# Kernel tuning notes

Measured on AMD Instinct MI355X. Metric: run time of the kernel, lower is better.

## Reference

```python
import jax, jax.numpy as jnp
import numpy as np

WS = 16          # window_size
OWS = 24         # overlap_win_size = int(ws*0.5) + ws
PAD = (OWS - WS) // 2
NH = 6           # num_heads


def _ln(x, g, b):
    m = jnp.mean(x, axis=-1, keepdims=True)
    v = jnp.mean((x - m) ** 2, axis=-1, keepdims=True)
    return (x - m) * jax.lax.rsqrt(v + 1e-5) * g + b


def setup_inputs() -> dict:
    key = jax.random.key(0)
    ks = jax.random.split(key, 12)
    B, H, W, C = 4, 64, 64, 180
    std = 0.02
    x = jax.random.normal(ks[0], (B, H * W, C), jnp.float32)
    y = jax.random.normal(ks[1], (B, H * W, C), jnp.float32)
    kv_w = jax.random.normal(ks[2], (2 * C, C), jnp.float32) * std
    kv_b = jnp.zeros((2 * C,), jnp.float32)
    q_w = jax.random.normal(ks[3], (C, C), jnp.float32) * std
    q_b = jnp.zeros((C,), jnp.float32)
    rpb = jax.random.normal(ks[4], ((WS + OWS - 1) ** 2, NH), jnp.float32) * std
    proj_w = jax.random.normal(ks[5], (C, C), jnp.float32) * std
    proj_b = jnp.zeros((C,), jnp.float32)
    fc1_w = jax.random.normal(ks[6], (4 * C, C), jnp.float32) * std
    fc1_b = jnp.zeros((4 * C,), jnp.float32)
    fc2_w = jax.random.normal(ks[7], (C, 4 * C), jnp.float32) * std
    fc2_b = jnp.zeros((C,), jnp.float32)
    norm1_g = jnp.ones((C,), jnp.float32); norm1_b = jnp.zeros((C,), jnp.float32)
    norm2_g = jnp.ones((C,), jnp.float32); norm2_b = jnp.zeros((C,), jnp.float32)
    # relative position index (HAT-style OCA): query coords vs extended window coords
    co = np.stack(np.meshgrid(np.arange(WS), np.arange(WS), indexing='ij')).reshape(2, -1)   # 2, ws*ws
    ce = np.stack(np.meshgrid(np.arange(OWS), np.arange(OWS), indexing='ij')).reshape(2, -1) # 2, ows*ows
    rel = (ce[:, None, :] - co[:, :, None]).transpose(1, 2, 0) + (WS - 1)  # nq, n, 2 in [0, ws+ows-2]
    rpi = jnp.asarray(rel[..., 0] * (WS + OWS - 1) + rel[..., 1], jnp.int32)  # [256, 576]
    return {
        'x': x, 'y': y,
        'norm1_g': norm1_g, 'norm1_b': norm1_b,
        'kv_w': kv_w, 'kv_b': kv_b, 'q_w': q_w, 'q_b': q_b,
        'rpb': rpb, 'proj_w': proj_w, 'proj_b': proj_b,
        'norm2_g': norm2_g, 'norm2_b': norm2_b,
        'fc1_w': fc1_w, 'fc1_b': fc1_b, 'fc2_w': fc2_w, 'fc2_b': fc2_b,
        'rpi': rpi, 'h': 64, 'w': 64,
    }


def reference(x, y, norm1_g, norm1_b, kv_w, kv_b, q_w, q_b, rpb, proj_w, proj_b,
              norm2_g, norm2_b, fc1_w, fc1_b, fc2_w, fc2_b, rpi, h, w):
    b, L, c = x.shape
    nh = NH
    d = c // nh
    scale = d ** -0.5
    nwh, nww = h // WS, w // WS
    nq, n = WS * WS, OWS * OWS

    shortcut = x
    xn = _ln(x, norm1_g, norm1_b).reshape(b, h, w, c)
    yn = _ln(y, norm1_g, norm1_b).reshape(b, h, w, c)

    kv = xn @ kv_w.T + kv_b                                  # b,h,w,2c
    q = yn @ q_w.T + q_b                                     # b,h,w,c

    # kv -> [2, b, c, h, w] then pad spatially and extract overlapping windows (nn.Unfold)
    kv = kv.reshape(b, h, w, 2, c).transpose(3, 0, 4, 1, 2)  # 2,b,c,h,w
    kvp = jnp.pad(kv, ((0, 0), (0, 0), (0, 0), (PAD, PAD), (PAD, PAD)))
    hh = jnp.arange(nwh)[:, None] * WS + jnp.arange(OWS)[None, :]   # [nwh, OWS]
    ww = jnp.arange(nww)[:, None] * WS + jnp.arange(OWS)[None, :]   # [nww, OWS]
    patches = kvp[:, :, :, hh][:, :, :, :, :, ww]            # 2,b,c,nwh,OWS,nww,OWS
    kvw = patches.transpose(0, 1, 3, 5, 4, 6, 2).reshape(2, b * nwh * nww, n, c)
    kwin, vwin = kvw[0], kvw[1]                              # [b_, n, c]

    # non-overlapping query windows (window_partition)
    qwin = q.reshape(b, nwh, WS, nww, WS, c).transpose(0, 1, 3, 2, 4, 5).reshape(-1, nq, c)
    b_ = qwin.shape[0]

    qh = qwin.reshape(b_, nq, nh, d).transpose(0, 2, 1, 3) * scale
    kh = kwin.reshape(b_, n, nh, d).transpose(0, 2, 1, 3)
    vh = vwin.reshape(b_, n, nh, d).transpose(0, 2, 1, 3)

    attn = jnp.einsum('bhqd,bhkd->bhqk', qh, kh)             # [b_, nh, nq, n]
    bias = rpb[rpi.reshape(-1)].reshape(nq, n, nh).transpose(2, 0, 1)  # [nh, nq, n]
    attn = jax.nn.softmax(attn + bias[None], axis=-1)
    out = jnp.einsum('bhqk,bhkd->bhqd', attn, vh).transpose(0, 2, 1, 3).reshape(b_, nq, c)

    # window_reverse
    out = out.reshape(b, nwh, nww, WS, WS, c).transpose(0, 1, 3, 2, 4, 5).reshape(b, h * w, c)

    xo = out @ proj_w.T + proj_b + shortcut
    xn2 = _ln(xo, norm2_g, norm2_b)
    mlp = jax.nn.gelu(xn2 @ fc1_w.T + fc1_b, approximate=False) @ fc2_w.T + fc2_b
    return xo + mlp
```

## Files before the change

kernel.cpp:

```cpp
#include <hip/hip_runtime.h>

typedef __bf16 bf16;
typedef __bf16 bf16x8 __attribute__((ext_vector_type(8)));
typedef __bf16 bf16x4 __attribute__((ext_vector_type(4)));
typedef __bf16 bf16x2 __attribute__((ext_vector_type(2)));
typedef float f32x4 __attribute__((ext_vector_type(4)));

static __device__ __forceinline__ bf16x8 ld8(const bf16* p) {
    return *reinterpret_cast<const bf16x8*>(p);
}
static __device__ __forceinline__ bf16x4 ld4(const bf16* p) {
    return *reinterpret_cast<const bf16x4*>(p);
}
static __device__ __forceinline__ bf16x8 ld8_b32(const bf16* p) {
    bf16x8 v;
#pragma unroll
    for (int i = 0; i < 4; ++i) {
        bf16x2 t = *reinterpret_cast<const bf16x2*>(p + i * 2);
        v[i * 2] = t[0]; v[i * 2 + 1] = t[1];
    }
    return v;
}
static __device__ __forceinline__ bf16x8 zero8() {
    bf16x8 v;
#pragma unroll
    for (int i = 0; i < 8; ++i) v[i] = (bf16)0.f;
    return v;
}

#define MFMA16(a, b, c) __builtin_amdgcn_mfma_f32_16x16x32_bf16((a), (b), (c), 0, 0, 0)

template <int BK, int KPAD>
static __device__ __forceinline__ void stage_tile(const bf16* __restrict__ g,
                                                  bf16* __restrict__ lds, int tid) {
    constexpr int CPR = BK / 8;
    constexpr int NP = 64 * CPR / 256;
#pragma unroll
    for (int p = 0; p < NP; ++p) {
        int idx = p * 256 + tid;
        int row = idx / CPR, cg = idx % CPR;
        bf16x8 v = ld8(g + (long)row * KPAD + cg * 8);
        *reinterpret_cast<bf16x8*>(lds + row * 200 + cg * 8) = v;
    }
}
template <int BK, int KPAD>
static __device__ __forceinline__ void load_chunk(const bf16* __restrict__ g,
                                                  bf16x8* r, int tid) {
    constexpr int CPR = BK / 8;
    constexpr int NP = 64 * CPR / 256;
#pragma unroll
    for (int p = 0; p < NP; ++p) {
        int idx = p * 256 + tid;
        int row = idx / CPR, cg = idx % CPR;
        r[p] = ld8(g + (long)row * KPAD + cg * 8);
    }
}
template <int BK>
static __device__ __forceinline__ void store_chunk(bf16* __restrict__ lds,
                                                   const bf16x8* r, int tid) {
    constexpr int CPR = BK / 8;
    constexpr int NP = 64 * CPR / 256;
#pragma unroll
    for (int p = 0; p < NP; ++p) {
        int idx = p * 256 + tid;
        int row = idx / CPR, cg = idx % CPR;
        *reinterpret_cast<bf16x8*>(lds + row * 200 + cg * 8) = r[p];
    }
}

__global__ __launch_bounds__(256) void prep_kernel(
    const float* __restrict__ kv_w, const float* __restrict__ q_w,
    const float* __restrict__ proj_w, const float* __restrict__ fc1_w,
    const float* __restrict__ fc2_w, const float* __restrict__ rpb,
    const int* __restrict__ rpi,
    bf16* __restrict__ wkv, bf16* __restrict__ wq, bf16* __restrict__ wproj,
    bf16* __restrict__ wfc1, bf16* __restrict__ wfc2, bf16* __restrict__ biast)
{
    int i = blockIdx.x * 256 + threadIdx.x;
    if (i < 73728) {
        int n = i / 192, k = i % 192;
        float v = (n < 360 && k < 180) ? kv_w[n * 180 + k] : 0.f;
        wkv[i] = (bf16)v;
    } else if (i < 122880) {
        int j = i - 73728; int n = j / 192, k = j % 192;
        float v = (n < 180 && k < 180) ? q_w[n * 180 + k] : 0.f;
        wq[j] = (bf16)v;
    } else if (i < 172032) {
        int j = i - 122880; int n = j / 192, k = j % 192;
        int hh = k >> 5, d = k & 31;
        float v = (n < 180 && d < 30) ? proj_w[n * 180 + hh * 30 + d] : 0.f;
        wproj[j] = (bf16)v;
    } else if (i < 319488) {
        int j = i - 172032; int n = j / 192, k = j % 192;
        float v = (n < 720 && k < 180) ? fc1_w[n * 180 + k] : 0.f;
        wfc1[j] = (bf16)v;
    } else if (i < 507904) {
        int j = i - 319488; int n = j / 736, k = j % 736;
        float v = (n < 180 && k < 720) ? fc2_w[n * 720 + k] : 0.f;
        wfc2[j] = (bf16)v;
    } else if (i < 1392640) {
        int t = i - 507904;
        int r = t & 3;
        int lane = (t >> 2) & 63;
        int tmp2 = t >> 8;
        int kg = tmp2 % 36;
        int tmp3 = tmp2 / 36;
        int qg = tmp3 & 15;
        int h = tmp3 >> 4;
        int q = qg * 16 + (lane & 15);
        int key = kg * 16 + ((lane >> 4) << 2) + r;
        biast[t] = (bf16)rpb[rpi[q * 576 + key] * 6 + h];
    }
}

__global__ __launch_bounds__(256) void ln_kernel(
    const float* __restrict__ srcA, const float* __restrict__ srcB,
    const float* __restrict__ g, const float* __restrict__ b,
    bf16* __restrict__ dst)
{
    int wave = threadIdx.x >> 6, lane = threadIdx.x & 63;
    int row = blockIdx.x * 4 + wave;
    const float* sp = (row < 16384) ? (srcA + row * 180) : (srcB + (row - 16384) * 180);
    float v0 = sp[lane];
    float v1 = sp[lane + 64];
    float v2 = (lane < 52) ? sp[lane + 128] : 0.f;
    float s = v0 + v1 + v2;
    float sq = v0 * v0 + v1 * v1 + v2 * v2;
#pragma unroll
    for (int m = 32; m >= 1; m >>= 1) {
        s += __shfl_xor(s, m);
        sq += __shfl_xor(sq, m);
    }
    float mean = s * (1.f / 180.f);
    float var = sq * (1.f / 180.f) - mean * mean;
    float rs = rsqrtf(var + 1e-5f);
    bf16* dp = dst + (long)row * 192;
    dp[lane] = (bf16)((v0 - mean) * rs * g[lane] + b[lane]);
    dp[lane + 64] = (bf16)((v1 - mean) * rs * g[lane + 64] + b[lane + 64]);
    float o2 = (lane < 52) ? ((v2 - mean) * rs * g[lane + 128] + b[lane + 128]) : 0.f;
    dp[lane + 128] = (bf16)o2;
}

__global__ __launch_bounds__(256, 4) void gemm_kvq(
    const bf16* __restrict__ xn, const bf16* __restrict__ yn,
    const bf16* __restrict__ wkv, const bf16* __restrict__ wq,
    const float* __restrict__ kv_b, const float* __restrict__ q_b,
    bf16* __restrict__ kvbuf, bf16* __restrict__ qbuf)
{
    const int tid = threadIdx.x, wave = tid >> 6, lane = tid & 63;
    const int llo = lane & 15, quad = lane >> 4;
    const int bz = blockIdx.y;
    const bool isq = (bz == 2);
    const bf16* A = isq ? yn : xn;
    const bf16* Wbase = isq ? wq : (wkv + (long)bz * 3 * 64 * 192);
    const int tm = blockIdx.x * 64;

    __shared__ __align__(16) bf16 Sa[64 * 200];
    __shared__ __align__(16) bf16 Sb[64 * 200];

    stage_tile<192, 192>(A + (long)tm * 192, Sa, tid);
    bf16x8 wreg[6];
    load_chunk<192, 192>(Wbase, wreg, tid);

    for (int s = 0; s < 3; ++s) {
        if (s) __syncthreads();
        store_chunk<192>(Sb, wreg, tid);
        __syncthreads();
        if (s < 2) load_chunk<192, 192>(Wbase + (long)(s + 1) * 64 * 192, wreg, tid);

        f32x4 acc[4];
#pragma unroll
        for (int nt = 0; nt < 4; ++nt)
#pragma unroll
            for (int r = 0; r < 4; ++r) acc[nt][r] = 0.f;
#pragma unroll
        for (int kt = 0; kt < 6; ++kt) {
            bf16x8 a = ld8(Sa + (wave * 16 + llo) * 200 + kt * 32 + quad * 8);
#pragma unroll
            for (int nt = 0; nt < 4; ++nt) {
                bf16x8 b = ld8(Sb + (nt * 16 + llo) * 200 + kt * 32 + quad * 8);
                acc[nt] = MFMA16(a, b, acc[nt]);
            }
        }

        const int g = bz * 3 + s;
#pragma unroll
        for (int nt = 0; nt < 4; ++nt)
#pragma unroll
            for (int r = 0; r < 4; ++r) {
                int m = tm + wave * 16 + quad * 4 + r;
                int n = g * 64 + nt * 16 + llo;
                if (!isq) {
                    if (n < 360) {
                        float v = acc[nt][r] + kv_b[n];
                        int nn = n % 180;
                        int col = (n / 180) * 192 + (nn / 30) * 32 + (nn % 30);
                        kvbuf[(long)m * 384 + col] = (bf16)v;
                    }
                } else {
                    int nq = n - 384;
                    if (nq < 180) {
                        float v = (acc[nt][r] + q_b[nq]) * 0.18257418583505537f;
                        int col = (nq / 30) * 32 + (nq % 30);
                        qbuf[(long)m * 192 + col] = (bf16)v;
                    }
                }
            }
    }
}

__global__ __launch_bounds__(512, 6) void attn_kernel(
    const bf16* __restrict__ qbuf,
    const bf16* __restrict__ kvbuf,
    const bf16* __restrict__ biast,
    bf16* __restrict__ obuf)
{
    const int qhalf = blockIdx.x & 1;
    const int head = (blockIdx.x >> 1) % 6;
    const int win = blockIdx.x / 12;
    const int bb = win / 16, wi = (win % 16) / 4, wj = win % 4;
    const int tid = threadIdx.x;
    const int wave = tid >> 6, lane = tid & 63;
    const int llo = lane & 15, quad = lane >> 4;
    const int qbase = qhalf * 128 + wave * 16;
    const int qg = qhalf * 8 + wave;

    __shared__ bf16 Kc[2][64][40];
    __shared__ bf16 Vt[2][32][74];
    __shared__ bf16 Ps[8][16][72];

    const int u = tid & 255;
    const int tloc = u >> 2, dq = u & 3;
    const bool isV = tid >= 256;
    int aa = tloc / 24, w0 = tloc % 24;

    const int q0 = qbase + llo;
    const int gr_q = bb * 4096 + (wi * 16 + (q0 >> 4)) * 64 + (wj * 16 + (q0 & 15));
    const bf16x8 qf = ld8(qbuf + (long)gr_q * 192 + head * 32 + quad * 8);
    const bf16* bbase = biast + ((long)(head * 16 + qg) * 36) * 256 + lane * 4;

    {
        int gy = wi * 16 + aa - 4, gx = wj * 16 + w0 - 4;
        bf16x8 st = zero8();
        if ((unsigned)gy < 64u && (unsigned)gx < 64u) {
            long gr = (long)(bb * 4096 + gy * 64 + gx) * 384;
            st = ld8(kvbuf + gr + (isV ? 192 : 0) + head * 32 + dq * 8);
        }
        if (!isV) {
            *reinterpret_cast<bf16x8*>(&Kc[0][tloc][dq * 8]) = st;
        } else {
#pragma unroll
            for (int j = 0; j < 8; ++j) Vt[0][dq * 8 + j][tloc] = st[j];
        }
    }
    __syncthreads();

    f32x4 o[2];
    float m_run = -1e30f, l_run = 0.f;
#pragma unroll
    for (int n2 = 0; n2 < 2; ++n2)
#pragma unroll
        for (int r = 0; r < 4; ++r) o[n2][r] = 0.f;

    for (int c = 0; c < 9; ++c) {
        const int cur = c & 1;

        bf16x8 stage;
        if (c < 8) {
            w0 += 16; aa += 2;
            if (w0 >= 24) { w0 -= 24; ++aa; }
            int gy = wi * 16 + aa - 4, gx = wj * 16 + w0 - 4;
            stage = zero8();
            if ((unsigned)gy < 64u && (unsigned)gx < 64u) {
                long gr = (long)(bb * 4096 + gy * 64 + gx) * 384;
                stage = ld8(kvbuf + gr + (isV ? 192 : 0) + head * 32 + dq * 8);
            }
        }

        f32x4 s[4];
#pragma unroll
        for (int kt = 0; kt < 4; ++kt) {
            bf16x8 kf = ld8(&Kc[cur][kt * 16 + llo][quad * 8]);
            f32x4 zc;
            zc[0] = 0.f; zc[1] = 0.f; zc[2] = 0.f; zc[3] = 0.f;
            s[kt] = MFMA16(kf, qf, zc);
        }

#pragma unroll
        for (int kt = 0; kt < 4; ++kt) {
            bf16x4 bv = ld4(bbase + (c * 4 + kt) * 256);
#pragma unroll
            for (int r = 0; r < 4; ++r) s[kt][r] += (float)bv[r];
        }

        float mx = s[0][0];
#pragma unroll
        for (int kt = 0; kt < 4; ++kt)
#pragma unroll
            for (int r = 0; r < 4; ++r) mx = fmaxf(mx, s[kt][r]);
        mx = fmaxf(mx, __shfl_xor(mx, 16));
        mx = fmaxf(mx, __shfl_xor(mx, 32));
        float m_new = fmaxf(m_run, mx);
        float alpha = __expf(m_run - m_new);
        float ls = 0.f;
#pragma unroll
        for (int kt = 0; kt < 4; ++kt)
#pragma unroll
            for (int r = 0; r < 4; ++r) {
                float p = __expf(s[kt][r] - m_new);
                s[kt][r] = p;
                ls += p;
            }
        ls += __shfl_xor(ls, 16);
        ls += __shfl_xor(ls, 32);
        l_run = l_run * alpha + ls;
        m_run = m_new;

#pragma unroll
        for (int r = 0; r < 4; ++r) {
            float a = __shfl(alpha, quad * 4 + r);
            o[0][r] *= a;
            o[1][r] *= a;
        }

#pragma unroll
        for (int kt = 0; kt < 4; ++kt) {
            bf16x4 pv;
#pragma unroll
            for (int r = 0; r < 4; ++r) pv[r] = (bf16)s[kt][r];
            *reinterpret_cast<bf16x4*>(&Ps[wave][llo][kt * 16 + quad * 4]) = pv;
        }

#pragma unroll
        for (int kt2 = 0; kt2 < 2; ++kt2) {
            bf16x8 pa = ld8(&Ps[wave][llo][kt2 * 32 + quad * 8]);
#pragma unroll
            for (int n2 = 0; n2 < 2; ++n2) {
                bf16x8 vb = ld8_b32(&Vt[cur][n2 * 16 + llo][kt2 * 32 + quad * 8]);
                o[n2] = MFMA16(pa, vb, o[n2]);
            }
        }

        if (c < 8) {
            if (!isV) {
                *reinterpret_cast<bf16x8*>(&Kc[1 - cur][tloc][dq * 8]) = stage;
            } else {
#pragma unroll
                for (int j = 0; j < 8; ++j) Vt[1 - cur][dq * 8 + j][tloc] = stage[j];
            }
            __syncthreads();
        }
    }

    float linv = 1.f / l_run;
#pragma unroll
    for (int r = 0; r < 4; ++r) {
        float li = __shfl(linv, quad * 4 + r);
        int q = qbase + quad * 4 + r;
        int gr = bb * 4096 + (wi * 16 + (q >> 4)) * 64 + (wj * 16 + (q & 15));
#pragma unroll
        for (int n2 = 0; n2 < 2; ++n2)
            obuf[(long)gr * 192 + head * 32 + n2 * 16 + llo] = (bf16)(o[n2][r] * li);
    }
}

__global__ __launch_bounds__(256, 3) void gemm_projln(
    const bf16* __restrict__ obuf, const bf16* __restrict__ wproj,
    const float* __restrict__ proj_b, const float* __restrict__ x,
    const float* __restrict__ g, const float* __restrict__ bln,
    float* __restrict__ xo, bf16* __restrict__ xn2)
{
    const int tid = threadIdx.x, wave = tid >> 6, lane = tid & 63;
    const int llo = lane & 15, quad = lane >> 4;
    const int mbase = blockIdx.x * 64;

    __shared__ __align__(16) bf16 Sa[64 * 200];
    __shared__ __align__(16) bf16 Sb[64 * 200];
    stage_tile<192, 192>(obuf + (long)mbase * 192, Sa, tid);
    bf16x8 wreg[6];
    load_chunk<192, 192>(wproj, wreg, tid);

    f32x4 acc[12];
#pragma unroll
    for (int nt = 0; nt < 12; ++nt)
#pragma unroll
        for (int r = 0; r < 4; ++r) acc[nt][r] = 0.f;

    for (int nc = 0; nc < 3; ++nc) {
        if (nc) __syncthreads();
        store_chunk<192>(Sb, wreg, tid);
        __syncthreads();
        if (nc < 2) load_chunk<192, 192>(wproj + (long)(nc + 1) * 64 * 192, wreg, tid);
#pragma unroll
        for (int kt = 0; kt < 6; ++kt) {
            bf16x8 a = ld8(Sa + (wave * 16 + llo) * 200 + kt * 32 + quad * 8);
#pragma unroll
            for (int nt = 0; nt < 4; ++nt) {
                bf16x8 b = ld8(Sb + (nt * 16 + llo) * 200 + kt * 32 + quad * 8);
                acc[nc * 4 + nt] = MFMA16(a, b, acc[nc * 4 + nt]);
            }
        }
    }

#pragma unroll
    for (int r = 0; r < 4; ++r) {
        int m = mbase + wave * 16 + quad * 4 + r;
        float v[12];
        float sum = 0.f, sq = 0.f;
#pragma unroll
        for (int nt = 0; nt < 12; ++nt) {
            int n = nt * 16 + llo;
            float val = 0.f;
            if (n < 180) val = acc[nt][r] + proj_b[n] + x[(long)m * 180 + n];
            v[nt] = val;
            sum += val; sq += val * val;
        }
#pragma unroll
        for (int msk = 1; msk <= 8; msk <<= 1) {
            sum += __shfl_xor(sum, msk);
            sq  += __shfl_xor(sq, msk);
        }
        float mean = sum * (1.f / 180.f);
        float var = sq * (1.f / 180.f) - mean * mean;
        float rs = rsqrtf(var + 1e-5f);
#pragma unroll
        for (int nt = 0; nt < 12; ++nt) {
            int n = nt * 16 + llo;
            if (n < 180) {
                xo[(long)m * 180 + n] = v[nt];
                xn2[(long)m * 192 + n] = (bf16)((v[nt] - mean) * rs * g[n] + bln[n]);
            } else {
                xn2[(long)m * 192 + n] = (bf16)0.f;
            }
        }
    }
}

__global__ __launch_bounds__(256, 4) void gemm_fc1(
    const bf16* __restrict__ A, const bf16* __restrict__ W,
    const float* __restrict__ bias, bf16* __restrict__ outp)
{
    const int tid = threadIdx.x, wave = tid >> 6, lane = tid & 63;
    const int llo = lane & 15, quad = lane >> 4;
    const int tm = blockIdx.x * 64;
    const int bz = blockIdx.y;
    const bf16* Wbase = W + (long)bz * 3 * 64 * 192;

    __shared__ __align__(16) bf16 Sa[64 * 200];
    __shared__ __align__(16) bf16 Sb[64 * 200];
    stage_tile<192, 192>(A + (long)tm * 192, Sa, tid);
    bf16x8 wreg[6];
    load_chunk<192, 192>(Wbase, wreg, tid);

    for (int s = 0; s < 3; ++s) {
        if (s) __syncthreads();
        store_chunk<192>(Sb, wreg, tid);
        __syncthreads();
        if (s < 2) load_chunk<192, 192>(Wbase + (long)(s + 1) * 64 * 192, wreg, tid);

        f32x4 acc[4];
#pragma unroll
        for (int nt = 0; nt < 4; ++nt)
#pragma unroll
            for (int r = 0; r < 4; ++r) acc[nt][r] = 0.f;
#pragma unroll
        for (int kt = 0; kt < 6; ++kt) {
            bf16x8 a = ld8(Sa + (wave * 16 + llo) * 200 + kt * 32 + quad * 8);
#pragma unroll
            for (int nt = 0; nt < 4; ++nt) {
                bf16x8 b = ld8(Sb + (nt * 16 + llo) * 200 + kt * 32 + quad * 8);
                acc[nt] = MFMA16(a, b, acc[nt]);
            }
        }

        const int nb = (bz * 3 + s) * 64;
#pragma unroll
        for (int nt = 0; nt < 4; ++nt)
#pragma unroll
            for (int r = 0; r < 4; ++r) {
                int m = tm + wave * 16 + quad * 4 + r;
                int n = nb + nt * 16 + llo;
                if (n >= 720) continue;
                float v = acc[nt][r] + bias[n];
                float gel = 0.5f * v * (1.f + erff(v * 0.7071067811865475f));
                outp[(long)m * 736 + n] = (bf16)gel;
            }
    }
}

__global__ __launch_bounds__(256, 4) void gemm_fc2(
    const bf16* __restrict__ A, const bf16* __restrict__ W,
    const float* __restrict__ bias, const float* __restrict__ resid,
    float* __restrict__ outp)
{
    const int tid = threadIdx.x, wave = tid >> 6, lane = tid & 63;
    const int llo = lane & 15, quad = lane >> 4;
    const int tm = blockIdx.x * 64;
    const int tn = blockIdx.y * 64;

    __shared__ __align__(16) bf16 Sa[64 * 200];
    __shared__ __align__(16) bf16 Sb[64 * 200];

    const bf16* Ap = A + (long)tm * 736;
    const bf16* Wp = W + (long)tn * 736;

    bf16x8 ar[6], wr[6];
    load_chunk<192, 736>(Ap, ar, tid);
    load_chunk<192, 736>(Wp, wr, tid);

    f32x4 acc[4];
#pragma unroll
    for (int nt = 0; nt < 4; ++nt)
#pragma unroll
        for (int r = 0; r < 4; ++r) acc[nt][r] = 0.f;

#pragma unroll
    for (int c = 0; c < 4; ++c) {
        if (c) __syncthreads();
        if (c < 3) { store_chunk<192>(Sa, ar, tid); store_chunk<192>(Sb, wr, tid); }
        else       { store_chunk<160>(Sa, ar, tid); store_chunk<160>(Sb, wr, tid); }
        __syncthreads();
        if (c < 2) {
            load_chunk<192, 736>(Ap + (c + 1) * 192, ar, tid);
            load_chunk<192, 736>(Wp + (c + 1) * 192, wr, tid);
        } else if (c == 2) {
            load_chunk<160, 736>(Ap + 576, ar, tid);
            load_chunk<160, 736>(Wp + 576, wr, tid);
        }
        const int nkt = (c == 3) ? 5 : 6;
        for (int kt = 0; kt < nkt; ++kt) {
            bf16x8 a = ld8(Sa + (wave * 16 + llo) * 200 + kt * 32 + quad * 8);
#pragma unroll
            for (int nt = 0; nt < 4; ++nt) {
                bf16x8 b = ld8(Sb + (nt * 16 + llo) * 200 + kt * 32 + quad * 8);
                acc[nt] = MFMA16(a, b, acc[nt]);
            }
        }
    }

#pragma unroll
    for (int nt = 0; nt < 4; ++nt)
#pragma unroll
        for (int r = 0; r < 4; ++r) {
            int m = tm + wave * 16 + quad * 4 + r;
            int n = tn + nt * 16 + llo;
            if (n >= 180) continue;
            float v = acc[nt][r] + bias[n];
            outp[(long)m * 180 + n] = v + resid[(long)m * 180 + n];
        }
}

extern "C" void kernel_launch(void* const* d_in, const int* in_sizes, int n_in,
                              void* d_out, int out_size, void* d_ws, size_t ws_size,
                              hipStream_t stream) {
    const float* x      = (const float*)d_in[0];
    const float* y      = (const float*)d_in[1];
    const float* n1g    = (const float*)d_in[2];
    const float* n1b    = (const float*)d_in[3];
    const float* kv_w   = (const float*)d_in[4];
    const float* kv_b   = (const float*)d_in[5];
    const float* q_w    = (const float*)d_in[6];
    const float* q_b    = (const float*)d_in[7];
    const float* rpb    = (const float*)d_in[8];
    const float* proj_w = (const float*)d_in[9];
    const float* proj_b = (const float*)d_in[10];
    const float* n2g    = (const float*)d_in[11];
    const float* n2b    = (const float*)d_in[12];
    const float* fc1_w  = (const float*)d_in[13];
    const float* fc1_b  = (const float*)d_in[14];
    const float* fc2_w  = (const float*)d_in[15];
    const float* fc2_b  = (const float*)d_in[16];
    const int*   rpi    = (const int*)d_in[17];

    char* ws = (char*)d_ws;
    bf16* xn    = (bf16*)(ws + 0);
    bf16* yn    = (bf16*)(ws + 6291456);
    bf16* qbuf  = (bf16*)(ws + 12582912);
    bf16* kvbuf = (bf16*)(ws + 18874368);
    bf16* obuf  = (bf16*)(ws + 31457280);
    float* xo   = (float*)(ws + 37748736);
    bf16* biast = (bf16*)(ws + 49545216);
    bf16* wkv   = (bf16*)(ws + 51314688);
    bf16* wq    = (bf16*)(ws + 51462144);
    bf16* wproj = (bf16*)(ws + 51560448);
    bf16* wfc1  = (bf16*)(ws + 51658752);
    bf16* wfc2  = (bf16*)(ws + 51953664);
    bf16* hmid  = (bf16*)(ws + 6291456);
    bf16* xn2   = xn;

    prep_kernel<<<5440, 256, 0, stream>>>(kv_w, q_w, proj_w, fc1_w, fc2_w, rpb, rpi,
                                          wkv, wq, wproj, wfc1, wfc2, biast);
    ln_kernel<<<8192, 256, 0, stream>>>(x, y, n1g, n1b, xn);
    gemm_kvq<<<dim3(256, 3), 256, 0, stream>>>(xn, yn, wkv, wq, kv_b, q_b, kvbuf, qbuf);
    attn_kernel<<<768, 512, 0, stream>>>(qbuf, kvbuf, biast, obuf);
    gemm_projln<<<256, 256, 0, stream>>>(obuf, wproj, proj_b, x, n2g, n2b, xo, xn2);
    gemm_fc1<<<dim3(256, 4), 256, 0, stream>>>(xn2, wfc1, fc1_b, hmid);
    gemm_fc2<<<dim3(256, 3), 256, 0, stream>>>(hmid, wfc2, fc2_b, xo, (float*)d_out);
}
```

Before: 211.9 us.

## Fuse LN into prep kernel and double M-tile for kvq and fc1 GEMMs

Merges the weight/bias prep kernel and the first layernorm kernel into one launch, removing a kernel launch. The kvq and fc1 GEMMs now use 512-thread blocks with 128-row A tiles, so each staged weight chunk is reused across twice as many rows and grid size halves. Bias loads in the epilogues are hoisted out of the per-row loop. The larger LDS footprint per block may lower occupancy.

```diff
diff --git a/kernel.cpp b/kernel.cpp
--- a/kernel.cpp
+++ b/kernel.cpp
@@ -30,45 +30,54 @@
 
 #define MFMA16(a, b, c) __builtin_amdgcn_mfma_f32_16x16x32_bf16((a), (b), (c), 0, 0, 0)
 
-template <int BK, int KPAD>
+template <int ROWS, int BK, int KPAD, int THREADS>
+static __device__ __forceinline__ void load_chunk_g(const bf16* __restrict__ g,
+                                                    bf16x8* r, int tid) {
+    constexpr int TOT = ROWS * BK / 8;
+    constexpr int NP = (TOT + THREADS - 1) / THREADS;
+#pragma unroll
+    for (int p = 0; p < NP; ++p) {
+        int idx = p * THREADS + tid;
+        if ((TOT % THREADS) == 0 || idx < TOT) {
+            int row = idx / (BK / 8), cg = idx % (BK / 8);
+            r[p] = ld8(g + (long)row * KPAD + cg * 8);
+        }
+    }
+}
+template <int ROWS, int BK, int THREADS>
+static __device__ __forceinline__ void store_chunk_l(bf16* __restrict__ lds,
+                                                     const bf16x8* r, int tid) {
+    constexpr int TOT = ROWS * BK / 8;
+    constexpr int NP = (TOT + THREADS - 1) / THREADS;
+#pragma unroll
+    for (int p = 0; p < NP; ++p) {
+        int idx = p * THREADS + tid;
+        if ((TOT % THREADS) == 0 || idx < TOT) {
+            int row = idx / (BK / 8), cg = idx % (BK / 8);
+            *reinterpret_cast<bf16x8*>(lds + row * 200 + cg * 8) = r[p];
+        }
+    }
+}
+template <int ROWS, int BK, int KPAD, int THREADS>
 static __device__ __forceinline__ void stage_tile(const bf16* __restrict__ g,
                                                   bf16* __restrict__ lds, int tid) {
-    constexpr int CPR = BK / 8;
-    constexpr int NP = 64 * CPR / 256;
+    constexpr int TOT = ROWS * BK / 8;
+    constexpr int NP = (TOT + THREADS - 1) / THREADS;
 #pragma unroll
     for (int p = 0; p < NP; ++p) {
-        int idx = p * 256 + tid;
-        int row = idx / CPR, cg = idx % CPR;
-        bf16x8 v = ld8(g + (long)row * KPAD + cg * 8);
-        *reinterpret_cast<bf16x8*>(lds + row * 200 + cg * 8) = v;
-    }
-}
-template <int BK, int KPAD>
-static __device__ __forceinline__ void load_chunk(const bf16* __restrict__ g,
-                                                  bf16x8* r, int tid) {
-    constexpr int CPR = BK / 8;
-    constexpr int NP = 64 * CPR / 256;
-#pragma unroll
-    for (int p = 0; p < NP; ++p) {
-        int idx = p * 256 + tid;
-        int row = idx / CPR, cg = idx % CPR;
-        r[p] = ld8(g + (long)row * KPAD + cg * 8);
-    }
-}
-template <int BK>
-static __device__ __forceinline__ void store_chunk(bf16* __restrict__ lds,
-                                                   const bf16x8* r, int tid) {
-    constexpr int CPR = BK / 8;
-    constexpr int NP = 64 * CPR / 256;
-#pragma unroll
-    for (int p = 0; p < NP; ++p) {
-        int idx = p * 256 + tid;
-        int row = idx / CPR, cg = idx % CPR;
-        *reinterpret_cast<bf16x8*>(lds + row * 200 + cg * 8) = r[p];
-    }
-}
-
-__global__ __launch_bounds__(256) void prep_kernel(
+        int idx = p * THREADS + tid;
+        if ((TOT % THREADS) == 0 || idx < TOT) {
+            int row = idx / (BK / 8), cg = idx % (BK / 8);
+            bf16x8 v = ld8(g + (long)row * KPAD + cg * 8);
+            *reinterpret_cast<bf16x8*>(lds + row * 200 + cg * 8) = v;
+        }
+    }
+}
+
+__global__ __launch_bounds__(256) void fused_pre(
+    const float* __restrict__ x, const float* __restrict__ y,
+    const float* __restrict__ g, const float* __restrict__ b,
+    bf16* __restrict__ dst,
     const float* __restrict__ kv_w, const float* __restrict__ q_w,
     const float* __restrict__ proj_w, const float* __restrict__ fc1_w,
     const float* __restrict__ fc2_w, const float* __restrict__ rpb,
@@ -76,7 +85,32 @@
     bf16* __restrict__ wkv, bf16* __restrict__ wq, bf16* __restrict__ wproj,
     bf16* __restrict__ wfc1, bf16* __restrict__ wfc2, bf16* __restrict__ biast)
 {
-    int i = blockIdx.x * 256 + threadIdx.x;
+    if (blockIdx.x < 8192) {
+        int wave = threadIdx.x >> 6, lane = threadIdx.x & 63;
+        int row = blockIdx.x * 4 + wave;
+        const float* sp = (row < 16384) ? (x + (long)row * 180)
+                                        : (y + (long)(row - 16384) * 180);
+        float v0 = sp[lane];
+        float v1 = sp[lane + 64];
+        float v2 = (lane < 52) ? sp[lane + 128] : 0.f;
+        float s = v0 + v1 + v2;
+        float sq = v0 * v0 + v1 * v1 + v2 * v2;
+#pragma unroll
+        for (int m = 32; m >= 1; m >>= 1) {
+            s += __shfl_xor(s, m);
+            sq += __shfl_xor(sq, m);
+        }
+        float mean = s * (1.f / 180.f);
+        float var = sq * (1.f / 180.f) - mean * mean;
+        float rs = rsqrtf(var + 1e-5f);
+        bf16* dp = dst + (long)row * 192;
+        dp[lane] = (bf16)((v0 - mean) * rs * g[lane] + b[lane]);
+        dp[lane + 64] = (bf16)((v1 - mean) * rs * g[lane + 64] + b[lane + 64]);
+        float o2 = (lane < 52) ? ((v2 - mean) * rs * g[lane + 128] + b[lane + 128]) : 0.f;
+        dp[lane + 128] = (bf16)o2;
+        return;
+    }
+    int i = (blockIdx.x - 8192) * 256 + threadIdx.x;
     if (i < 73728) {
         int n = i / 192, k = i % 192;
         float v = (n < 360 && k < 180) ? kv_w[n * 180 + k] : 0.f;
@@ -113,35 +147,7 @@
     }
 }
 
-__global__ __launch_bounds__(256) void ln_kernel(
-    const float* __restrict__ srcA, const float* __restrict__ srcB,
-    const float* __restrict__ g, const float* __restrict__ b,
-    bf16* __restrict__ dst)
-{
-    int wave = threadIdx.x >> 6, lane = threadIdx.x & 63;
-    int row = blockIdx.x * 4 + wave;
-    const float* sp = (row < 16384) ? (srcA + row * 180) : (srcB + (row - 16384) * 180);
-    float v0 = sp[lane];
-    float v1 = sp[lane + 64];
-    float v2 = (lane < 52) ? sp[lane + 128] : 0.f;
-    float s = v0 + v1 + v2;
-    float sq = v0 * v0 + v1 * v1 + v2 * v2;
-#pragma unroll
-    for (int m = 32; m >= 1; m >>= 1) {
-        s += __shfl_xor(s, m);
-        sq += __shfl_xor(sq, m);
-    }
-    float mean = s * (1.f / 180.f);
-    float var = sq * (1.f / 180.f) - mean * mean;
-    float rs = rsqrtf(var + 1e-5f);
-    bf16* dp = dst + (long)row * 192;
-    dp[lane] = (bf16)((v0 - mean) * rs * g[lane] + b[lane]);
-    dp[lane + 64] = (bf16)((v1 - mean) * rs * g[lane + 64] + b[lane + 64]);
-    float o2 = (lane < 52) ? ((v2 - mean) * rs * g[lane + 128] + b[lane + 128]) : 0.f;
-    dp[lane + 128] = (bf16)o2;
-}
-
-__global__ __launch_bounds__(256, 4) void gemm_kvq(
+__global__ __launch_bounds__(512, 4) void gemm_kvq(
     const bf16* __restrict__ xn, const bf16* __restrict__ yn,
     const bf16* __restrict__ wkv, const bf16* __restrict__ wq,
     const float* __restrict__ kv_b, const float* __restrict__ q_b,
@@ -153,20 +159,20 @@
     const bool isq = (bz == 2);
     const bf16* A = isq ? yn : xn;
     const bf16* Wbase = isq ? wq : (wkv + (long)bz * 3 * 64 * 192);
-    const int tm = blockIdx.x * 64;
-
-    __shared__ __align__(16) bf16 Sa[64 * 200];
+    const int tm = blockIdx.x * 128;
+
+    __shared__ __align__(16) bf16 Sa[128 * 200];
     __shared__ __align__(16) bf16 Sb[64 * 200];
 
-    stage_tile<192, 192>(A + (long)tm * 192, Sa, tid);
-    bf16x8 wreg[6];
-    load_chunk<192, 192>(Wbase, wreg, tid);
+    stage_tile<128, 192, 192, 512>(A + (long)tm * 192, Sa, tid);
+    bf16x8 wreg[3];
+    load_chunk_g<64, 192, 192, 512>(Wbase, wreg, tid);
 
     for (int s = 0; s < 3; ++s) {
         if (s) __syncthreads();
-        store_chunk<192>(Sb, wreg, tid);
+        store_chunk_l<64, 192, 512>(Sb, wreg, tid);
         __syncthreads();
-        if (s < 2) load_chunk<192, 192>(Wbase + (long)(s + 1) * 64 * 192, wreg, tid);
+        if (s < 2) load_chunk_g<64, 192, 192, 512>(Wbase + (long)(s + 1) * 64 * 192, wreg, tid);
 
         f32x4 acc[4];
 #pragma unroll
@@ -185,35 +191,39 @@
 
         const int g = bz * 3 + s;
 #pragma unroll
-        for (int nt = 0; nt < 4; ++nt)
-#pragma unroll
-            for (int r = 0; r < 4; ++r) {
-                int m = tm + wave * 16 + quad * 4 + r;
-                int n = g * 64 + nt * 16 + llo;
-                if (!isq) {
-                    if (n < 360) {
-                        float v = acc[nt][r] + kv_b[n];
-                        int nn = n % 180;
-                        int col = (n / 180) * 192 + (nn / 30) * 32 + (nn % 30);
-                        kvbuf[(long)m * 384 + col] = (bf16)v;
-                    }
-                } else {
-                    int nq = n - 384;
-                    if (nq < 180) {
-                        float v = (acc[nt][r] + q_b[nq]) * 0.18257418583505537f;
-                        int col = (nq / 30) * 32 + (nq % 30);
-                        qbuf[(long)m * 192 + col] = (bf16)v;
+        for (int nt = 0; nt < 4; ++nt) {
+            int n = g * 64 + nt * 16 + llo;
+            if (!isq) {
+                if (n < 360) {
+                    int nn = n % 180;
+                    int col = (n / 180) * 192 + (nn / 30) * 32 + (nn % 30);
+                    float bv = kv_b[n];
+#pragma unroll
+                    for (int r = 0; r < 4; ++r) {
+                        int m = tm + wave * 16 + quad * 4 + r;
+                        kvbuf[(long)m * 384 + col] = (bf16)(acc[nt][r] + bv);
                     }
                 }
-            }
+            } else {
+                int nq = n - 384;
+                if (nq < 180) {
+                    int col = (nq / 30) * 32 + (nq % 30);
+                    float bv = q_b[nq];
+#pragma unroll
+                    for (int r = 0; r < 4; ++r) {
+                        int m = tm + wave * 16 + quad * 4 + r;
+                        qbuf[(long)m * 192 + col] =
+                            (bf16)((acc[nt][r] + bv) * 0.18257418583505537f);
+                    }
+                }
+            }
+        }
     }
 }
 
 __global__ __launch_bounds__(512, 6) void attn_kernel(
-    const bf16* __restrict__ qbuf,
-    const bf16* __restrict__ kvbuf,
-    const bf16* __restrict__ biast,
-    bf16* __restrict__ obuf)
+    const bf16* __restrict__ qbuf, const bf16* __restrict__ kvbuf,
+    const bf16* __restrict__ biast, bf16* __restrict__ obuf)
 {
     const int qhalf = blockIdx.x & 1;
     const int head = (blockIdx.x >> 1) % 6;
@@ -376,9 +386,9 @@
 
     __shared__ __align__(16) bf16 Sa[64 * 200];
     __shared__ __align__(16) bf16 Sb[64 * 200];
-    stage_tile<192, 192>(obuf + (long)mbase * 192, Sa, tid);
+    stage_tile<64, 192, 192, 256>(obuf + (long)mbase * 192, Sa, tid);
     bf16x8 wreg[6];
-    load_chunk<192, 192>(wproj, wreg, tid);
+    load_chunk_g<64, 192, 192, 256>(wproj, wreg, tid);
 
     f32x4 acc[12];
 #pragma unroll
@@ -388,9 +398,9 @@
 
     for (int nc = 0; nc < 3; ++nc) {
         if (nc) __syncthreads();
-        store_chunk<192>(Sb, wreg, tid);
+        store_chunk_l<64, 192, 256>(Sb, wreg, tid);
         __syncthreads();
-        if (nc < 2) load_chunk<192, 192>(wproj + (long)(nc + 1) * 64 * 192, wreg, tid);
+        if (nc < 2) load_chunk_g<64, 192, 192, 256>(wproj + (long)(nc + 1) * 64 * 192, wreg, tid);
 #pragma unroll
         for (int kt = 0; kt < 6; ++kt) {
             bf16x8 a = ld8(Sa + (wave * 16 + llo) * 200 + kt * 32 + quad * 8);
@@ -436,27 +446,27 @@
     }
 }
 
-__global__ __launch_bounds__(256, 4) void gemm_fc1(
+__global__ __launch_bounds__(512, 4) void gemm_fc1(
     const bf16* __restrict__ A, const bf16* __restrict__ W,
     const float* __restrict__ bias, bf16* __restrict__ outp)
 {
     const int tid = threadIdx.x, wave = tid >> 6, lane = tid & 63;
     const int llo = lane & 15, quad = lane >> 4;
-    const int tm = blockIdx.x * 64;
+    const int tm = blockIdx.x * 128;
     const int bz = blockIdx.y;
     const bf16* Wbase = W + (long)bz * 3 * 64 * 192;
 
-    __shared__ __align__(16) bf16 Sa[64 * 200];
+    __shared__ __align__(16) bf16 Sa[128 * 200];
     __shared__ __align__(16) bf16 Sb[64 * 200];
-    stage_tile<192, 192>(A + (long)tm * 192, Sa, tid);
-    bf16x8 wreg[6];
-    load_chunk<192, 192>(Wbase, wreg, tid);
+    stage_tile<128, 192, 192, 512>(A + (long)tm * 192, Sa, tid);
+    bf16x8 wreg[3];
+    load_chunk_g<64, 192, 192, 512>(Wbase, wreg, tid);
 
     for (int s = 0; s < 3; ++s) {
         if (s) __syncthreads();
-        store_chunk<192>(Sb, wreg, tid);
+        store_chunk_l<64, 192, 512>(Sb, wreg, tid);
         __syncthreads();
-        if (s < 2) load_chunk<192, 192>(Wbase + (long)(s + 1) * 64 * 192, wreg, tid);
+        if (s < 2) load_chunk_g<64, 192, 192, 512>(Wbase + (long)(s + 1) * 64 * 192, wreg, tid);
 
         f32x4 acc[4];
 #pragma unroll
@@ -475,16 +485,18 @@
 
         const int nb = (bz * 3 + s) * 64;
 #pragma unroll
-        for (int nt = 0; nt < 4; ++nt)
+        for (int nt = 0; nt < 4; ++nt) {
+            int n = nb + nt * 16 + llo;
+            if (n >= 720) continue;
+            float bv = bias[n];
 #pragma unroll
             for (int r = 0; r < 4; ++r) {
                 int m = tm + wave * 16 + quad * 4 + r;
-                int n = nb + nt * 16 + llo;
-                if (n >= 720) continue;
-                float v = acc[nt][r] + bias[n];
+                float v = acc[nt][r] + bv;
                 float gel = 0.5f * v * (1.f + erff(v * 0.7071067811865475f));
                 outp[(long)m * 736 + n] = (bf16)gel;
             }
+        }
     }
 }
 
@@ -505,8 +517,8 @@
     const bf16* Wp = W + (long)tn * 736;
 
     bf16x8 ar[6], wr[6];
-    load_chunk<192, 736>(Ap, ar, tid);
-    load_chunk<192, 736>(Wp, wr, tid);
+    load_chunk_g<64, 192, 736, 256>(Ap, ar, tid);
+    load_chunk_g<64, 192, 736, 256>(Wp, wr, tid);
 
     f32x4 acc[4];
 #pragma unroll
@@ -517,15 +529,20 @@
 #pragma unroll
     for (int c = 0; c < 4; ++c) {
         if (c) __syncthreads();
-        if (c < 3) { store_chunk<192>(Sa, ar, tid); store_chunk<192>(Sb, wr, tid); }
-        else       { store_chunk<160>(Sa, ar, tid); store_chunk<160>(Sb, wr, tid); }
+        if (c < 3) {
+            store_chunk_l<64, 192, 256>(Sa, ar, tid);
+            store_chunk_l<64, 192, 256>(Sb, wr, tid);
+        } else {
+            store_chunk_l<64, 160, 256>(Sa, ar, tid);
+            store_chunk_l<64, 160, 256>(Sb, wr, tid);
+        }
         __syncthreads();
         if (c < 2) {
-            load_chunk<192, 736>(Ap + (c + 1) * 192, ar, tid);
-            load_chunk<192, 736>(Wp + (c + 1) * 192, wr, tid);
+            load_chunk_g<64, 192, 736, 256>(Ap + (c + 1) * 192, ar, tid);
+            load_chunk_g<64, 192, 736, 256>(Wp + (c + 1) * 192, wr, tid);
         } else if (c == 2) {
-            load_chunk<160, 736>(Ap + 576, ar, tid);
-            load_chunk<160, 736>(Wp + 576, wr, tid);
+            load_chunk_g<64, 160, 736, 256>(Ap + 576, ar, tid);
+            load_chunk_g<64, 160, 736, 256>(Wp + 576, wr, tid);
         }
         const int nkt = (c == 3) ? 5 : 6;
         for (int kt = 0; kt < nkt; ++kt) {
@@ -588,12 +605,12 @@
     bf16* hmid  = (bf16*)(ws + 6291456);
     bf16* xn2   = xn;
 
-    prep_kernel<<<5440, 256, 0, stream>>>(kv_w, q_w, proj_w, fc1_w, fc2_w, rpb, rpi,
-                                          wkv, wq, wproj, wfc1, wfc2, biast);
-    ln_kernel<<<8192, 256, 0, stream>>>(x, y, n1g, n1b, xn);
-    gemm_kvq<<<dim3(256, 3), 256, 0, stream>>>(xn, yn, wkv, wq, kv_b, q_b, kvbuf, qbuf);
+    fused_pre<<<13632, 256, 0, stream>>>(x, y, n1g, n1b, xn,
+                                         kv_w, q_w, proj_w, fc1_w, fc2_w, rpb, rpi,
+                                         wkv, wq, wproj, wfc1, wfc2, biast);
+    gemm_kvq<<<dim3(128, 3), 512, 0, stream>>>(xn, yn, wkv, wq, kv_b, q_b, kvbuf, qbuf);
     attn_kernel<<<768, 512, 0, stream>>>(qbuf, kvbuf, biast, obuf);
     gemm_projln<<<256, 256, 0, stream>>>(obuf, wproj, proj_b, x, n2g, n2b, xo, xn2);
-    gemm_fc1<<<dim3(256, 4), 256, 0, stream>>>(xn2, wfc1, fc1_b, hmid);
+    gemm_fc1<<<dim3(128, 4), 512, 0, stream>>>(xn2, wfc1, fc1_b, hmid);
     gemm_fc2<<<dim3(256, 3), 256, 0, stream>>>(hmid, wfc2, fc2_b, xo, (float*)d_out);
 }
```

Result: faster. 201.6 us (-4.8%).
